# Performance work log

Measured on AMD Instinct MI355X. Metric: run time of the kernel, lower is better.

The kernel has to match this reference:

```python
import jax, jax.numpy as jnp
import numpy as np

N_NODES = 100000
N_EDGES = 1600000
N_REL = 2
IN_CH, HID_CH, OUT_CH = 128, 128, 64


def setup_inputs() -> dict:
    key = jax.random.key(0)
    ks = jax.random.split(key, 8)
    x = jax.random.normal(ks[0], (N_NODES, IN_CH), dtype=jnp.float32)
    edge_index = jax.random.randint(ks[1], (2, N_EDGES), 0, N_NODES, dtype=jnp.int64)
    edge_type = jax.random.randint(ks[2], (N_EDGES,), 0, N_REL, dtype=jnp.int64)
    s1 = 1.0 / np.sqrt(IN_CH)
    s2 = 1.0 / np.sqrt(HID_CH)
    W1_rel = jax.random.normal(ks[3], (N_REL, IN_CH, HID_CH), dtype=jnp.float32) * s1
    W1_root = jax.random.normal(ks[4], (IN_CH, HID_CH), dtype=jnp.float32) * s1
    b1 = jnp.zeros((HID_CH,), dtype=jnp.float32)
    W2_rel = jax.random.normal(ks[5], (N_REL, HID_CH, OUT_CH), dtype=jnp.float32) * s2
    W2_root = jax.random.normal(ks[6], (HID_CH, OUT_CH), dtype=jnp.float32) * s2
    b2 = jnp.zeros((OUT_CH,), dtype=jnp.float32)
    return {"x": x, "edge_index": edge_index, "edge_type": edge_type,
            "W1_rel": W1_rel, "W1_root": W1_root, "b1": b1,
            "W2_rel": W2_rel, "W2_root": W2_root, "b2": b2}


def rgcn_conv(x, edge_index, edge_type, W_rel, W_root, b):
    """Relational graph conv: root transform + per-relation gather/matmul/scatter-mean."""
    src, dst = edge_index[0], edge_index[1]
    N = x.shape[0]
    out = x @ W_root + b  # self/root term
    x_src = x[src]  # [E, in] gather once, reused across relations
    for r in range(W_rel.shape[0]):  # N_REL is small and fixed
        mask = (edge_type == r)
        msg = jnp.where(mask[:, None], x_src, 0.0) @ W_rel[r]  # [E, out]
        agg = jax.ops.segment_sum(msg, dst, num_segments=N)  # [N, out]
        cnt = jax.ops.segment_sum(mask.astype(x.dtype), dst, num_segments=N)
        out = out + agg / jnp.maximum(cnt, 1.0)[:, None]  # mean aggregation
    return out


def l2_normalize(x, eps=1e-12):
    nrm = jnp.sqrt(jnp.sum(x * x, axis=1, keepdims=True))
    return x / jnp.maximum(nrm, eps)


def reference(x, edge_index, edge_type, W1_rel, W1_root, b1, W2_rel, W2_root, b2):
    h = jax.nn.relu(rgcn_conv(x, edge_index, edge_type, W1_rel, W1_root, b1))
    out = rgcn_conv(h, edge_index, edge_type, W2_rel, W2_root, b2)
    return l2_normalize(out)
```

## Files before the change

kernel.cpp:

```cpp
#include <hip/hip_runtime.h>
#include <hip/hip_bf16.h>


typedef unsigned int uint;
typedef unsigned short ushort;
typedef __attribute__((ext_vector_type(8))) short short8;
typedef __attribute__((ext_vector_type(16))) float floatx16;
typedef __attribute__((ext_vector_type(2))) float f32x2;
typedef __attribute__((ext_vector_type(4))) float f32x4;
typedef __attribute__((ext_vector_type(4))) uint u32x4;

#define IN_CH  128
#define OUT_CH 64
#define SCAN_CHUNK 2048
#define EPB 8192
#define KPB 512
#define MAXBK 400

__device__ __forceinline__ ushort f2bf(float f) {
    uint u = __float_as_uint(f);
    u += 0x7FFF + ((u >> 16) & 1);
    return (ushort)(u >> 16);
}
__device__ __forceinline__ float bflo(uint u) { return __uint_as_float(u << 16); }
__device__ __forceinline__ float bfhi(uint u) { return __uint_as_float(u & 0xFFFF0000u); }


__global__ void k_scan_a(const int* __restrict__ deg, int* __restrict__ offs,
                         int* __restrict__ bsums, int n) {
    __shared__ int sdata[256];
    int b = blockIdx.x, t = threadIdx.x;
    int base = b * SCAN_CHUNK + t * 8;
    int v[8];
    int sum = 0;
#pragma unroll
    for (int i = 0; i < 8; i++) {
        int idx = base + i;
        int x = (idx < n) ? deg[idx] : 0;
        v[i] = sum;
        sum += x;
    }
    sdata[t] = sum;
    __syncthreads();
    for (int ofs = 1; ofs < 256; ofs <<= 1) {
        int val = sdata[t];
        int add = (t >= ofs) ? sdata[t - ofs] : 0;
        __syncthreads();
        sdata[t] = val + add;
        __syncthreads();
    }
    int texcl = (t == 0) ? 0 : sdata[t - 1];
    if (t == 255) bsums[b] = sdata[255];
#pragma unroll
    for (int i = 0; i < 8; i++) {
        int idx = base + i;
        if (idx < n) offs[idx] = texcl + v[i];
    }
}

__global__ void k_scan_b(int* __restrict__ bsums, int* __restrict__ offs, int nb, int n) {
    int t = threadIdx.x;
    if (nb <= 64) {
        int v = (t < nb) ? bsums[t] : 0;
        int s = v;
#pragma unroll
        for (int d = 1; d < 64; d <<= 1) {
            int u = __shfl_up(s, d, 64);
            if (t >= d) s += u;
        }
        if (t < nb) bsums[t] = s - v;
        if (t == 63) offs[n] = s;
    } else if (t == 0) {
        int run = 0;
        for (int b = 0; b < nb; b++) {
            int x = bsums[b];
            bsums[b] = run;
            run += x;
        }
        offs[n] = run;
    }
}

__global__ void k_part(const int* __restrict__ src, const int* __restrict__ dst,
                       const int* __restrict__ et, const int* __restrict__ basebb,
                       const int* __restrict__ bsums,
                       uint* __restrict__ stage, int E, int NBK, int NBLK) {
    __shared__ int cnt[MAXBK];
    __shared__ int basel[MAXBK];
    int tid = threadIdx.x, blk = blockIdx.x;
    for (int b = tid; b < NBK; b += 256) {
        cnt[b] = 0;
        int i = b * NBLK + blk;
        basel[b] = basebb[i] + bsums[i >> 11];
    }
    __syncthreads();
    int base = blk * EPB;
#pragma unroll 4
    for (int i = 0; i < EPB / 256; i++) {
        int e = base + i * 256 + tid;
        if (e < E) {
            int s = src[e];
            int key = 2 * dst[e] + et[e];
            int bk = key >> 9;
            int r = atomicAdd(&cnt[bk], 1);
            stage[basel[bk] + r] = ((uint)(key & 511) << 23) | (uint)s;
        }
    }
}

__global__ void k_fine(const uint* __restrict__ stage, const int* __restrict__ basebb,
                       const int* __restrict__ bsums,
                       int* __restrict__ offs, int* __restrict__ esrc,
                       int E, int NBK, int NBLK) {
    __shared__ int kcnt[KPB];
    __shared__ int kcur[KPB];
    __shared__ int ssum[256];
    int tid = threadIdx.x, b = blockIdx.x;
    int i0 = b * NBLK;
    int start = basebb[i0] + bsums[i0 >> 11];
    int endB = E;
    if (b != NBK - 1) {
        int i1 = (b + 1) * NBLK;
        endB = basebb[i1] + bsums[i1 >> 11];
    }
    int size = endB - start;

    kcnt[tid] = 0;
    kcnt[tid + 256] = 0;
    __syncthreads();
    for (int i = tid; i < size; i += 256)
        atomicAdd(&kcnt[stage[start + i] >> 23], 1);
    __syncthreads();
    int v0 = kcnt[2 * tid], v1 = kcnt[2 * tid + 1];
    ssum[tid] = v0 + v1;
    __syncthreads();
    for (int ofs = 1; ofs < 256; ofs <<= 1) {
        int val = ssum[tid];
        int add = (tid >= ofs) ? ssum[tid - ofs] : 0;
        __syncthreads();
        ssum[tid] = val + add;
        __syncthreads();
    }
    int texcl = (tid == 0) ? 0 : ssum[tid - 1];
    kcur[2 * tid] = texcl;
    kcur[2 * tid + 1] = texcl + v0;
    offs[(b << 9) + 2 * tid] = start + texcl + v0;
    offs[(b << 9) + 2 * tid + 1] = start + texcl + v0 + v1;
    __syncthreads();
    for (int i = tid; i < size; i += 256) {
        uint p = stage[start + i];
        int r = atomicAdd(&kcur[p >> 23], 1);
        esrc[start + r] = (int)(p & 0x7FFFFFu);
    }
}


__device__ __forceinline__ uint4 pack8(const ushort* o) {
    uint4 v;
    v.x = (uint)o[0] | ((uint)o[1] << 16);
    v.y = (uint)o[2] | ((uint)o[3] << 16);
    v.z = (uint)o[4] | ((uint)o[5] << 16);
    v.w = (uint)o[6] | ((uint)o[7] << 16);
    return v;
}

__global__ void k_pre(const int* __restrict__ dst, const int* __restrict__ et,
                      int* __restrict__ cntblk, int E, int NBK, int NBLK,
                      const float* __restrict__ x, uint4* __restrict__ xb, int n8,
                      const float* __restrict__ W1root, const float* __restrict__ W1rel,
                      const float* __restrict__ W2root, const float* __restrict__ W2rel,
                      uint4* __restrict__ Bpk1, uint4* __restrict__ Bpk2,
                      uint* __restrict__ xzero, uint* __restrict__ t2zero) {
    __shared__ int cnt[MAXBK];
    int tid = threadIdx.x;
    if ((int)blockIdx.x < NBLK) {
        int blk = blockIdx.x;
        for (int b = tid; b < NBK; b += 256) cnt[b] = 0;
        __syncthreads();
        int base = blk * EPB;
#pragma unroll 4
        for (int i = 0; i < EPB / 256; i++) {
            int e = base + i * 256 + tid;
            if (e < E) {
                int key = 2 * dst[e] + et[e];
                atomicAdd(&cnt[key >> 9], 1);
            }
        }
        __syncthreads();
        for (int b = tid; b < NBK; b += 256) cntblk[b * NBLK + blk] = cnt[b];
        return;
    }
    int bid = blockIdx.x - NBLK;
    if (bid < 40) {
        if (bid == 0) {
            if (tid < 64) xzero[tid] = 0;
            if (tid < 96) t2zero[tid] = 0;
        }
        int idx = bid * 256 + tid;
        ushort o[8];
        if (idx < 6144) {
            int id = idx;
            int ct = id >> 11;
            int c = id & 2047;
            int gn = c >> 9, s = (c >> 6) & 7, h = (c >> 5) & 1, n = c & 31;
            int k0 = s * 16 + h * 8;
            int col = gn * 32 + n;
            const float* W = (ct == 0) ? W1root : (W1rel + (size_t)(ct - 1) * 16384);
#pragma unroll
            for (int j = 0; j < 8; j++) o[j] = f2bf(W[(k0 + j) * 128 + col]);
            Bpk1[id] = pack8(o);
        } else {
            int id = idx - 6144;
            int ct = id >> 11;
            int c = id & 2047;
            int gn = c >> 9, s = (c >> 6) & 7, h = (c >> 5) & 1, n = c & 31;
            int k0 = s * 16 + h * 8;
            int colg = ct * 128 + gn * 32 + n;
#pragma unroll
            for (int j = 0; j < 8; j++) {
                float f = 0.f;
                if (colg < 64)       f = W2root[(k0 + j) * 64 + colg];
                else if (colg < 128) f = W2rel[(k0 + j) * 64 + (colg - 64)];
                else if (colg < 192) f = W2rel[8192 + (k0 + j) * 64 + (colg - 128)];
                o[j] = f2bf(f);
            }
            Bpk2[id] = pack8(o);
        }
    } else {
        int i = (bid - 40) * 256 + tid;
        if (i >= n8) return;
        const f32x4* xp = (const f32x4*)x;
        f32x4 f0 = __builtin_nontemporal_load(&xp[(size_t)i * 2]);
        f32x4 f1 = __builtin_nontemporal_load(&xp[(size_t)i * 2 + 1]);
        uint4 o;
        o.x = (uint)f2bf(f0.x) | ((uint)f2bf(f0.y) << 16);
        o.y = (uint)f2bf(f0.z) | ((uint)f2bf(f0.w) << 16);
        o.z = (uint)f2bf(f1.x) | ((uint)f2bf(f1.y) << 16);
        o.w = (uint)f2bf(f1.z) | ((uint)f2bf(f1.w) << 16);
        xb[i] = o;
    }
}


__global__ __launch_bounds__(256)
void k_agg(const int* __restrict__ offs, const int* __restrict__ esrc,
           const uint4* __restrict__ xb4, uint* __restrict__ S, int N) {
    int wid = (int)((blockIdx.x * 256L + threadIdx.x) >> 5);
    int l = threadIdx.x & 31;
    if (wid >= N) return;
    int q = l >> 4, c = l & 15;

    int beg0 = (wid == 0) ? 0 : offs[2 * wid - 1];
    int end0 = offs[2 * wid], end1 = offs[2 * wid + 1];

    u32x4 o = {0, 0, 0, 0};
#pragma unroll
    for (int r = 0; r < 2; r++) {
        int beg = r ? end0 : beg0;
        int end = r ? end1 : end0;
        f32x2 a0 = {0.f, 0.f}, a1 = {0.f, 0.f}, a2 = {0.f, 0.f}, a3 = {0.f, 0.f};
        for (int c0 = beg; c0 < end; c0 += 32) {
            int myid = (c0 + l < end) ? __builtin_nontemporal_load(&esrc[c0 + l]) : N;
            int m = min(32, end - c0);
            for (int eb = 0; eb < m; eb += 4) {
#pragma unroll
                for (int j = 0; j < 2; j++) {
                    int id = __shfl(myid, eb + 2 * j + q, 32);
                    uint4 v = xb4[(uint)id * 16u + (uint)c];
                    a0 += (f32x2){bflo(v.x), bfhi(v.x)};
                    a1 += (f32x2){bflo(v.y), bfhi(v.y)};
                    a2 += (f32x2){bflo(v.z), bfhi(v.z)};
                    a3 += (f32x2){bflo(v.w), bfhi(v.w)};
                }
            }
        }
        a0.x += __shfl_xor(a0.x, 16, 32); a0.y += __shfl_xor(a0.y, 16, 32);
        a1.x += __shfl_xor(a1.x, 16, 32); a1.y += __shfl_xor(a1.y, 16, 32);
        a2.x += __shfl_xor(a2.x, 16, 32); a2.y += __shfl_xor(a2.y, 16, 32);
        a3.x += __shfl_xor(a3.x, 16, 32); a3.y += __shfl_xor(a3.y, 16, 32);
        if (q == r) {
            float inv = (end > beg) ? 1.0f / (float)(end - beg) : 0.f;
            o.x = (uint)f2bf(a0.x * inv) | ((uint)f2bf(a0.y * inv) << 16);
            o.y = (uint)f2bf(a1.x * inv) | ((uint)f2bf(a1.y * inv) << 16);
            o.z = (uint)f2bf(a2.x * inv) | ((uint)f2bf(a2.y * inv) << 16);
            o.w = (uint)f2bf(a3.x * inv) | ((uint)f2bf(a3.y * inv) << 16);
        }
    }
    u32x4* Sp = (u32x4*)S;
    __builtin_nontemporal_store(o, &Sp[(size_t)wid * 32 + q * 16 + c]);
}


__global__ __launch_bounds__(256)
void k_fused(const ushort* __restrict__ xb, const ushort* __restrict__ S1,
             const ushort* __restrict__ Bpk1, const float* __restrict__ b1,
             const ushort* __restrict__ Bpk2, ushort* __restrict__ Out, int N) {
    __shared__ ushort SH[40960];
    ushort* Alds = SH;
    ushort* Blds = SH + 16384;

    const int tid = threadIdx.x;
    const int lane = tid & 63;
    const int w = tid >> 6;
    const int wm = w >> 1, wn = w & 1;
    const int rowBase = blockIdx.x * 128;

    floatx16 acc[2][2] = {};

#pragma unroll
    for (int seg = 0; seg < 3; seg++) {
        const ushort* Ap = (seg == 0) ? xb : S1;
        const int stride = (seg == 0) ? 128 : 256;
        const int aoff = (seg == 2) ? 128 : 0;
        const uint4* Bsrc = (const uint4*)Bpk1 + seg * 2048;
#pragma unroll
        for (int i = 0; i < 8; i++) {
            int c = tid + i * 256;
            int m = c & 31, hh = (c >> 5) & 1, s = (c >> 6) & 7, g = c >> 9;
            int row = rowBase + g * 32 + m;
            if (row >= N) row = N - 1;
            int kc = s * 2 + hh;
            ((uint4*)Alds)[c] = *(const uint4*)(Ap + (size_t)row * stride + aoff + kc * 8);
            ((uint4*)Blds)[c] = Bsrc[c];
        }
        __syncthreads();
#pragma unroll
        for (int s = 0; s < 8; s++) {
            short8 a0 = *(const short8*)&Alds[(((wm * 2 + 0) * 8 + s) * 64 + lane) * 8];
            short8 a1 = *(const short8*)&Alds[(((wm * 2 + 1) * 8 + s) * 64 + lane) * 8];
            short8 b0 = *(const short8*)&Blds[(((wn * 2 + 0) * 8 + s) * 64 + lane) * 8];
            short8 b1f = *(const short8*)&Blds[(((wn * 2 + 1) * 8 + s) * 64 + lane) * 8];
            acc[0][0] = __builtin_amdgcn_mfma_f32_32x32x16_bf16(a0, b0, acc[0][0], 0, 0, 0);
            acc[0][1] = __builtin_amdgcn_mfma_f32_32x32x16_bf16(a0, b1f, acc[0][1], 0, 0, 0);
            acc[1][0] = __builtin_amdgcn_mfma_f32_32x32x16_bf16(a1, b0, acc[1][0], 0, 0, 0);
            acc[1][1] = __builtin_amdgcn_mfma_f32_32x32x16_bf16(a1, b1f, acc[1][1], 0, 0, 0);
        }
        __syncthreads();
    }

    {
        const int qr = 4 * (lane >> 5);
        const int cl = lane & 31;
        float bb[2];
#pragma unroll
        for (int nt = 0; nt < 2; nt++) bb[nt] = b1[wn * 64 + nt * 32 + cl];
#pragma unroll
        for (int mt = 0; mt < 2; mt++)
#pragma unroll
            for (int nt = 0; nt < 2; nt++) {
                int col = wn * 64 + nt * 32 + cl;
                int kc = col >> 3, j = col & 7;
                int s = kc >> 1, hh = kc & 1;
                int base = (((wm * 2 + mt) * 8 + s) * 64 + hh * 32) * 8 + j;
#pragma unroll
                for (int reg = 0; reg < 16; reg++) {
                    int rl = (reg & 3) + 8 * (reg >> 2) + qr;
                    float v = fmaxf(acc[mt][nt][reg] + bb[nt], 0.f);
                    Alds[base + rl * 8] = f2bf(v);
                }
            }
    }
    {
        const uint4* B2 = (const uint4*)Bpk2;
#pragma unroll
        for (int i = 0; i < 12; i++) {
            int c = tid + i * 256;
            ((uint4*)Blds)[c] = B2[c];
        }
    }
    __syncthreads();

    floatx16 acc2[2][3] = {};
#pragma unroll
    for (int s = 0; s < 8; s++) {
        short8 a0 = *(const short8*)&Alds[(((wm * 2 + 0) * 8 + s) * 64 + lane) * 8];
        short8 a1 = *(const short8*)&Alds[(((wm * 2 + 1) * 8 + s) * 64 + lane) * 8];
        short8 b0 = *(const short8*)&Blds[((wn * 3 + 0) * 512 + s * 64 + lane) * 8];
        short8 b1v = *(const short8*)&Blds[((wn * 3 + 1) * 512 + s * 64 + lane) * 8];
        short8 b2v = *(const short8*)&Blds[((wn * 3 + 2) * 512 + s * 64 + lane) * 8];
        acc2[0][0] = __builtin_amdgcn_mfma_f32_32x32x16_bf16(a0, b0, acc2[0][0], 0, 0, 0);
        acc2[0][1] = __builtin_amdgcn_mfma_f32_32x32x16_bf16(a0, b1v, acc2[0][1], 0, 0, 0);
        acc2[0][2] = __builtin_amdgcn_mfma_f32_32x32x16_bf16(a0, b2v, acc2[0][2], 0, 0, 0);
        acc2[1][0] = __builtin_amdgcn_mfma_f32_32x32x16_bf16(a1, b0, acc2[1][0], 0, 0, 0);
        acc2[1][1] = __builtin_amdgcn_mfma_f32_32x32x16_bf16(a1, b1v, acc2[1][1], 0, 0, 0);
        acc2[1][2] = __builtin_amdgcn_mfma_f32_32x32x16_bf16(a1, b2v, acc2[1][2], 0, 0, 0);
    }
    __syncthreads();

    ushort* Clds = SH;
    {
        const int qr = 4 * (lane >> 5);
        const int cl = lane & 31;
#pragma unroll
        for (int mt = 0; mt < 2; mt++)
#pragma unroll
            for (int nt = 0; nt < 3; nt++) {
#pragma unroll
                for (int reg = 0; reg < 16; reg++) {
                    int rl = (reg & 3) + 8 * (reg >> 2) + qr;
                    Clds[(wm * 64 + mt * 32 + rl) * 200 + wn * 96 + nt * 32 + cl] =
                        f2bf(acc2[mt][nt][reg]);
                }
            }
    }
    __syncthreads();

    int r = tid >> 1, half = tid & 1;
    int grow = rowBase + r;
    if (grow < N) {
#pragma unroll
        for (int k = 0; k < 12; k++) {
            int c0 = half * 96 + k * 8;
            uint4 v = *(const uint4*)&Clds[r * 200 + c0];
            *(uint4*)(Out + (size_t)grow * 192 + c0) = v;
        }
    }
}


__global__ __launch_bounds__(256)
void k_final(const ushort* __restrict__ T2, const float* __restrict__ b2,
             const int* __restrict__ offs, const int* __restrict__ esrc,
             float* __restrict__ out, int N) {
    int wid = (int)((blockIdx.x * 256L + threadIdx.x) >> 3);
    int c = threadIdx.x & 7;
    if (wid >= N) return;
    const uint4* Tb = (const uint4*)T2;

    int beg0 = (wid == 0) ? 0 : offs[2 * wid - 1];
    int end0 = offs[2 * wid], end1 = offs[2 * wid + 1];

    f32x2 t0 = {0.f, 0.f}, t1 = {0.f, 0.f}, t2v = {0.f, 0.f}, t3v = {0.f, 0.f};
#pragma unroll
    for (int r = 0; r < 2; r++) {
        int beg = r ? end0 : beg0;
        int end = r ? end1 : end0;
        if (end > beg) {
            f32x2 a0 = {0.f, 0.f}, a1 = {0.f, 0.f}, a2 = {0.f, 0.f}, a3 = {0.f, 0.f};
            uint bc = 8u + 8u * (uint)r + (uint)c;
            for (int c0 = beg; c0 < end; c0 += 8) {
                int myid = (c0 + c < end) ? __builtin_nontemporal_load(&esrc[c0 + c]) : N;
                int m = min(8, end - c0);
                for (int eb = 0; eb < m; eb += 4) {
                    uint4 v[4];
#pragma unroll
                    for (int j = 0; j < 4; j++) {
                        int id = __shfl(myid, eb + j, 8);
                        v[j] = Tb[(uint)id * 24u + bc];
                    }
#pragma unroll
                    for (int j = 0; j < 4; j++) {
                        a0 += (f32x2){bflo(v[j].x), bfhi(v[j].x)};
                        a1 += (f32x2){bflo(v[j].y), bfhi(v[j].y)};
                        a2 += (f32x2){bflo(v[j].z), bfhi(v[j].z)};
                        a3 += (f32x2){bflo(v[j].w), bfhi(v[j].w)};
                    }
                }
            }
            float inv = 1.0f / (float)(end - beg);
            t0 += a0 * inv; t1 += a1 * inv; t2v += a2 * inv; t3v += a3 * inv;
        }
    }
    uint4 ru = Tb[(uint)wid * 24u + (uint)c];
    float4 bbA = *(const float4*)(b2 + 8 * c);
    float4 bbB = *(const float4*)(b2 + 8 * c + 4);
    float v0 = bflo(ru.x) + bbA.x + t0.x;
    float v1 = bfhi(ru.x) + bbA.y + t0.y;
    float v2 = bflo(ru.y) + bbA.z + t1.x;
    float v3 = bfhi(ru.y) + bbA.w + t1.y;
    float v4 = bflo(ru.z) + bbB.x + t2v.x;
    float v5 = bfhi(ru.z) + bbB.y + t2v.y;
    float v6 = bflo(ru.w) + bbB.z + t3v.x;
    float v7 = bfhi(ru.w) + bbB.w + t3v.y;
    float sq = v0 * v0 + v1 * v1 + v2 * v2 + v3 * v3
             + v4 * v4 + v5 * v5 + v6 * v6 + v7 * v7;
#pragma unroll
    for (int d = 1; d <= 4; d <<= 1) sq += __shfl_xor(sq, d, 8);
    float rn = 1.0f / fmaxf(sqrtf(sq), 1e-12f);
    f32x4 oA = {v0 * rn, v1 * rn, v2 * rn, v3 * rn};
    f32x4 oB = {v4 * rn, v5 * rn, v6 * rn, v7 * rn};
    f32x4* op = (f32x4*)(out + (size_t)wid * 64 + 8 * c);
    __builtin_nontemporal_store(oA, op);
    __builtin_nontemporal_store(oB, op + 1);
}


extern "C" void kernel_launch(void* const* d_in, const int* in_sizes, int n_in,
                              void* d_out, int out_size, void* d_ws, size_t ws_size,
                              hipStream_t stream) {
    const float* x      = (const float*)d_in[0];
    const int*   ei     = (const int*)d_in[1];
    const int*   etype  = (const int*)d_in[2];
    const float* W1rel  = (const float*)d_in[3];
    const float* W1root = (const float*)d_in[4];
    const float* b1     = (const float*)d_in[5];
    const float* W2rel  = (const float*)d_in[6];
    const float* W2root = (const float*)d_in[7];
    const float* b2     = (const float*)d_in[8];
    float* out = (float*)d_out;

    const int N = in_sizes[0] / IN_CH;
    const int E = in_sizes[2];
    const int NKEY = 2 * N;
    const int NBK  = (NKEY + KPB - 1) / KPB;
    const int NBLK = (E + EPB - 1) / EPB;
    const int NSC  = NBK * NBLK;

    const int* src = ei;
    const int* dst = ei + E;

    char* base = (char*)d_ws;
    size_t off = 0;
    auto carve = [&](size_t bytes) -> void* {
        void* p = base + off;
        off = (off + bytes + 511) & ~(size_t)511;
        return p;
    };
    ushort* xb    = (ushort*)carve((size_t)(N + 1) * 128 * sizeof(ushort));
    ushort* S1    = (ushort*)carve((size_t)N * 256 * sizeof(ushort));
    ushort* t2    = (ushort*)carve((size_t)(N + 1) * 192 * sizeof(ushort));
    int*    esrc  = (int*)carve((size_t)E * sizeof(int));
    uint*   stage = (uint*)carve((size_t)E * sizeof(uint));
    int*    offs  = (int*)carve((size_t)NBK * KPB * sizeof(int));
    int*    cntblk= (int*)carve((size_t)NSC * sizeof(int));
    int*    basebb= (int*)carve((size_t)(NSC + 1) * sizeof(int));
    int     NB    = (NSC + SCAN_CHUNK - 1) / SCAN_CHUNK;
    int*    bsums = (int*)carve((size_t)NB * sizeof(int));
    uint4*  Bpk1  = (uint4*)carve(6144 * sizeof(uint4));
    uint4*  Bpk2  = (uint4*)carve(4096 * sizeof(uint4));
    (void)ws_size; (void)n_in; (void)out_size;

    int n8 = N * 16;
    int preBlocks = NBLK + 40 + (n8 + 255) / 256;

    k_pre<<<preBlocks, 256, 0, stream>>>(dst, etype, cntblk, E, NBK, NBLK,
                                         x, (uint4*)xb, n8,
                                         W1root, W1rel, W2root, W2rel,
                                         Bpk1, Bpk2,
                                         (uint*)(xb + (size_t)N * 128),
                                         (uint*)(t2 + (size_t)N * 192));

    k_scan_a<<<NB, 256, 0, stream>>>(cntblk, basebb, bsums, NSC);
    k_scan_b<<<1, 64, 0, stream>>>(bsums, basebb, NB, NSC);
    k_part<<<NBLK, 256, 0, stream>>>(src, dst, etype, basebb, bsums, stage, E, NBK, NBLK);
    k_fine<<<NBK, 256, 0, stream>>>(stage, basebb, bsums, offs, esrc, E, NBK, NBLK);

    int rowTiles = (N + 127) / 128;
    int aggBlocks = (N + 7) / 8;
    int finBlocks = (N + 31) / 32;

    k_agg<<<aggBlocks, 256, 0, stream>>>(offs, esrc, (const uint4*)xb, (uint*)S1, N);
    k_fused<<<rowTiles, 256, 0, stream>>>(xb, S1, (const ushort*)Bpk1, b1,
                                          (const ushort*)Bpk2, t2, N);

    k_final<<<finBlocks, 256, 0, stream>>>(t2, b2, offs, esrc, out, N);
}
```

Before: 330.9 us.

## Read weight fragments from global memory and shrink fused kernel LDS footprint

The fused GEMM kernel no longer stages the packed weight matrices in LDS. Each wave reads its B fragments straight from global memory, where they should stay hot in cache since every block shares them. The output tile is now written back in two 64-row halves so it fits in a 32 KB LDS buffer, down from 80 KB. This is meant to allow more resident blocks per CU and to drop the B staging copies, at the cost of global loads on the MFMA path and extra barriers during writeback.

```diff
diff --git a/kernel.cpp b/kernel.cpp
--- a/kernel.cpp
+++ b/kernel.cpp
@@ -295,9 +295,8 @@
 void k_fused(const ushort* __restrict__ xb, const ushort* __restrict__ S1,
              const ushort* __restrict__ Bpk1, const float* __restrict__ b1,
              const ushort* __restrict__ Bpk2, ushort* __restrict__ Out, int N) {
-    __shared__ ushort SH[40960];
+    __shared__ ushort SH[16384];
     ushort* Alds = SH;
-    ushort* Blds = SH + 16384;
 
     const int tid = threadIdx.x;
     const int lane = tid & 63;
@@ -305,6 +304,9 @@
     const int wm = w >> 1, wn = w & 1;
     const int rowBase = blockIdx.x * 128;
 
+    const short8* B1 = (const short8*)Bpk1;
+    const short8* B2 = (const short8*)Bpk2;
+
     floatx16 acc[2][2] = {};
 
 #pragma unroll
@@ -312,7 +314,6 @@
         const ushort* Ap = (seg == 0) ? xb : S1;
         const int stride = (seg == 0) ? 128 : 256;
         const int aoff = (seg == 2) ? 128 : 0;
-        const uint4* Bsrc = (const uint4*)Bpk1 + seg * 2048;
 #pragma unroll
         for (int i = 0; i < 8; i++) {
             int c = tid + i * 256;
@@ -321,15 +322,14 @@
             if (row >= N) row = N - 1;
             int kc = s * 2 + hh;
             ((uint4*)Alds)[c] = *(const uint4*)(Ap + (size_t)row * stride + aoff + kc * 8);
-            ((uint4*)Blds)[c] = Bsrc[c];
         }
         __syncthreads();
 #pragma unroll
         for (int s = 0; s < 8; s++) {
             short8 a0 = *(const short8*)&Alds[(((wm * 2 + 0) * 8 + s) * 64 + lane) * 8];
             short8 a1 = *(const short8*)&Alds[(((wm * 2 + 1) * 8 + s) * 64 + lane) * 8];
-            short8 b0 = *(const short8*)&Blds[(((wn * 2 + 0) * 8 + s) * 64 + lane) * 8];
-            short8 b1f = *(const short8*)&Blds[(((wn * 2 + 1) * 8 + s) * 64 + lane) * 8];
+            short8 b0 = B1[seg * 2048 + ((wn * 2 + 0) * 8 + s) * 64 + lane];
+            short8 b1f = B1[seg * 2048 + ((wn * 2 + 1) * 8 + s) * 64 + lane];
             acc[0][0] = __builtin_amdgcn_mfma_f32_32x32x16_bf16(a0, b0, acc[0][0], 0, 0, 0);
             acc[0][1] = __builtin_amdgcn_mfma_f32_32x32x16_bf16(a0, b1f, acc[0][1], 0, 0, 0);
             acc[1][0] = __builtin_amdgcn_mfma_f32_32x32x16_bf16(a1, b0, acc[1][0], 0, 0, 0);
@@ -360,14 +360,6 @@
                 }
             }
     }
-    {
-        const uint4* B2 = (const uint4*)Bpk2;
-#pragma unroll
-        for (int i = 0; i < 12; i++) {
-            int c = tid + i * 256;
-            ((uint4*)Blds)[c] = B2[c];
-        }
-    }
     __syncthreads();
 
     floatx16 acc2[2][3] = {};
@@ -375,9 +367,9 @@
     for (int s = 0; s < 8; s++) {
         short8 a0 = *(const short8*)&Alds[(((wm * 2 + 0) * 8 + s) * 64 + lane) * 8];
         short8 a1 = *(const short8*)&Alds[(((wm * 2 + 1) * 8 + s) * 64 + lane) * 8];
-        short8 b0 = *(const short8*)&Blds[((wn * 3 + 0) * 512 + s * 64 + lane) * 8];
-        short8 b1v = *(const short8*)&Blds[((wn * 3 + 1) * 512 + s * 64 + lane) * 8];
-        short8 b2v = *(const short8*)&Blds[((wn * 3 + 2) * 512 + s * 64 + lane) * 8];
+        short8 b0 = B2[((wn * 3 + 0) * 8 + s) * 64 + lane];
+        short8 b1v = B2[((wn * 3 + 1) * 8 + s) * 64 + lane];
+        short8 b2v = B2[((wn * 3 + 2) * 8 + s) * 64 + lane];
         acc2[0][0] = __builtin_amdgcn_mfma_f32_32x32x16_bf16(a0, b0, acc2[0][0], 0, 0, 0);
         acc2[0][1] = __builtin_amdgcn_mfma_f32_32x32x16_bf16(a0, b1v, acc2[0][1], 0, 0, 0);
         acc2[0][2] = __builtin_amdgcn_mfma_f32_32x32x16_bf16(a0, b2v, acc2[0][2], 0, 0, 0);
@@ -385,34 +377,36 @@
         acc2[1][1] = __builtin_amdgcn_mfma_f32_32x32x16_bf16(a1, b1v, acc2[1][1], 0, 0, 0);
         acc2[1][2] = __builtin_amdgcn_mfma_f32_32x32x16_bf16(a1, b2v, acc2[1][2], 0, 0, 0);
     }
-    __syncthreads();
 
     ushort* Clds = SH;
-    {
-        const int qr = 4 * (lane >> 5);
-        const int cl = lane & 31;
-#pragma unroll
-        for (int mt = 0; mt < 2; mt++)
-#pragma unroll
-            for (int nt = 0; nt < 3; nt++) {
-#pragma unroll
-                for (int reg = 0; reg < 16; reg++) {
-                    int rl = (reg & 3) + 8 * (reg >> 2) + qr;
-                    Clds[(wm * 64 + mt * 32 + rl) * 200 + wn * 96 + nt * 32 + cl] =
-                        f2bf(acc2[mt][nt][reg]);
+    const int qr = 4 * (lane >> 5);
+    const int cl = lane & 31;
+#pragma unroll
+    for (int half = 0; half < 2; half++) {
+        __syncthreads();
+        if (wm == half) {
+#pragma unroll
+            for (int mt = 0; mt < 2; mt++)
+#pragma unroll
+                for (int nt = 0; nt < 3; nt++) {
+#pragma unroll
+                    for (int reg = 0; reg < 16; reg++) {
+                        int rl = (reg & 3) + 8 * (reg >> 2) + qr;
+                        Clds[(mt * 32 + rl) * 200 + wn * 96 + nt * 32 + cl] =
+                            f2bf(acc2[mt][nt][reg]);
+                    }
                 }
+        }
+        __syncthreads();
+        int r = tid >> 2, q4 = tid & 3;
+        int grow = rowBase + half * 64 + r;
+        if (grow < N) {
+#pragma unroll
+            for (int k = 0; k < 6; k++) {
+                int c0 = q4 * 48 + k * 8;
+                uint4 v = *(const uint4*)&Clds[r * 200 + c0];
+                *(uint4*)(Out + (size_t)grow * 192 + c0) = v;
             }
-    }
-    __syncthreads();
-
-    int r = tid >> 1, half = tid & 1;
-    int grow = rowBase + r;
-    if (grow < N) {
-#pragma unroll
-        for (int k = 0; k < 12; k++) {
-            int c0 = half * 96 + k * 8;
-            uint4 v = *(const uint4*)&Clds[r * 200 + c0];
-            *(uint4*)(Out + (size_t)grow * 192 + c0) = v;
         }
     }
 }
```

Measured after the change: 338.3 us. 2.2% more time.

## Use 8 waves per block in fused GEMM kernel and plain stores in aggregation

Applied to the files above, without the earlier changes.

The fused two-layer GEMM kernel now launches 512 threads (8 waves) per 128-row tile. Each wave owns one 32-row M tile instead of two, which halves per-wave accumulators and MFMA work and spreads the LDS loads across more threads. This aims to raise latency hiding and reduce register pressure, at the cost of more A-fragment LDS reads relative to compute. The aggregation kernel also switches its S1 output from a nontemporal store to a normal store, so the data may stay in cache for the following fused kernel.

```diff
diff --git a/kernel.cpp b/kernel.cpp
--- a/kernel.cpp
+++ b/kernel.cpp
@@ -244,7 +244,7 @@
 
 __global__ __launch_bounds__(256)
 void k_agg(const int* __restrict__ offs, const int* __restrict__ esrc,
-           const uint4* __restrict__ xb4, uint* __restrict__ S, int N) {
+           const uint4* __restrict__ xb4, uint4* __restrict__ S4, int N) {
     int wid = (int)((blockIdx.x * 256L + threadIdx.x) >> 5);
     int l = threadIdx.x & 31;
     if (wid >= N) return;
@@ -253,7 +253,7 @@
     int beg0 = (wid == 0) ? 0 : offs[2 * wid - 1];
     int end0 = offs[2 * wid], end1 = offs[2 * wid + 1];
 
-    u32x4 o = {0, 0, 0, 0};
+    uint4 o = make_uint4(0, 0, 0, 0);
 #pragma unroll
     for (int r = 0; r < 2; r++) {
         int beg = r ? end0 : beg0;
@@ -286,12 +286,11 @@
             o.w = (uint)f2bf(a3.x * inv) | ((uint)f2bf(a3.y * inv) << 16);
         }
     }
-    u32x4* Sp = (u32x4*)S;
-    __builtin_nontemporal_store(o, &Sp[(size_t)wid * 32 + q * 16 + c]);
-}
-
-
-__global__ __launch_bounds__(256)
+    S4[(size_t)wid * 32 + q * 16 + c] = o;
+}
+
+
+__global__ __launch_bounds__(512)
 void k_fused(const ushort* __restrict__ xb, const ushort* __restrict__ S1,
              const ushort* __restrict__ Bpk1, const float* __restrict__ b1,
              const ushort* __restrict__ Bpk2, ushort* __restrict__ Out, int N) {
@@ -302,10 +301,11 @@
     const int tid = threadIdx.x;
     const int lane = tid & 63;
     const int w = tid >> 6;
-    const int wm = w >> 1, wn = w & 1;
+    const int wm = w & 3;
+    const int wn = w >> 2;
     const int rowBase = blockIdx.x * 128;
 
-    floatx16 acc[2][2] = {};
+    floatx16 acc[2] = {};
 
 #pragma unroll
     for (int seg = 0; seg < 3; seg++) {
@@ -314,8 +314,8 @@
         const int aoff = (seg == 2) ? 128 : 0;
         const uint4* Bsrc = (const uint4*)Bpk1 + seg * 2048;
 #pragma unroll
-        for (int i = 0; i < 8; i++) {
-            int c = tid + i * 256;
+        for (int i = 0; i < 4; i++) {
+            int c = tid + i * 512;
             int m = c & 31, hh = (c >> 5) & 1, s = (c >> 6) & 7, g = c >> 9;
             int row = rowBase + g * 32 + m;
             if (row >= N) row = N - 1;
@@ -326,14 +326,11 @@
         __syncthreads();
 #pragma unroll
         for (int s = 0; s < 8; s++) {
-            short8 a0 = *(const short8*)&Alds[(((wm * 2 + 0) * 8 + s) * 64 + lane) * 8];
-            short8 a1 = *(const short8*)&Alds[(((wm * 2 + 1) * 8 + s) * 64 + lane) * 8];
+            short8 a0 = *(const short8*)&Alds[((wm * 8 + s) * 64 + lane) * 8];
             short8 b0 = *(const short8*)&Blds[(((wn * 2 + 0) * 8 + s) * 64 + lane) * 8];
             short8 b1f = *(const short8*)&Blds[(((wn * 2 + 1) * 8 + s) * 64 + lane) * 8];
-            acc[0][0] = __builtin_amdgcn_mfma_f32_32x32x16_bf16(a0, b0, acc[0][0], 0, 0, 0);
-            acc[0][1] = __builtin_amdgcn_mfma_f32_32x32x16_bf16(a0, b1f, acc[0][1], 0, 0, 0);
-            acc[1][0] = __builtin_amdgcn_mfma_f32_32x32x16_bf16(a1, b0, acc[1][0], 0, 0, 0);
-            acc[1][1] = __builtin_amdgcn_mfma_f32_32x32x16_bf16(a1, b1f, acc[1][1], 0, 0, 0);
+            acc[0] = __builtin_amdgcn_mfma_f32_32x32x16_bf16(a0, b0, acc[0], 0, 0, 0);
+            acc[1] = __builtin_amdgcn_mfma_f32_32x32x16_bf16(a0, b1f, acc[1], 0, 0, 0);
         }
         __syncthreads();
     }
@@ -341,49 +338,39 @@
     {
         const int qr = 4 * (lane >> 5);
         const int cl = lane & 31;
-        float bb[2];
-#pragma unroll
-        for (int nt = 0; nt < 2; nt++) bb[nt] = b1[wn * 64 + nt * 32 + cl];
-#pragma unroll
-        for (int mt = 0; mt < 2; mt++)
-#pragma unroll
-            for (int nt = 0; nt < 2; nt++) {
-                int col = wn * 64 + nt * 32 + cl;
-                int kc = col >> 3, j = col & 7;
-                int s = kc >> 1, hh = kc & 1;
-                int base = (((wm * 2 + mt) * 8 + s) * 64 + hh * 32) * 8 + j;
-#pragma unroll
-                for (int reg = 0; reg < 16; reg++) {
-                    int rl = (reg & 3) + 8 * (reg >> 2) + qr;
-                    float v = fmaxf(acc[mt][nt][reg] + bb[nt], 0.f);
-                    Alds[base + rl * 8] = f2bf(v);
-                }
+#pragma unroll
+        for (int nt = 0; nt < 2; nt++) {
+            float bb = b1[wn * 64 + nt * 32 + cl];
+            int col = wn * 64 + nt * 32 + cl;
+            int kc = col >> 3, j = col & 7;
+            int s = kc >> 1, hh = kc & 1;
+            int base = ((wm * 8 + s) * 64 + hh * 32) * 8 + j;
+#pragma unroll
+            for (int reg = 0; reg < 16; reg++) {
+                int rl = (reg & 3) + 8 * (reg >> 2) + qr;
+                float v = fmaxf(acc[nt][reg] + bb, 0.f);
+                Alds[base + rl * 8] = f2bf(v);
             }
-    }
-    {
-        const uint4* B2 = (const uint4*)Bpk2;
-#pragma unroll
-        for (int i = 0; i < 12; i++) {
-            int c = tid + i * 256;
-            ((uint4*)Blds)[c] = B2[c];
-        }
-    }
-    __syncthreads();
-
-    floatx16 acc2[2][3] = {};
+        }
+        const uint4* B2s = (const uint4*)Bpk2;
+#pragma unroll
+        for (int i = 0; i < 6; i++) {
+            int c = tid + i * 512;
+            ((uint4*)Blds)[c] = B2s[c];
+        }
+    }
+    __syncthreads();
+
+    floatx16 acc2[3] = {};
 #pragma unroll
     for (int s = 0; s < 8; s++) {
-        short8 a0 = *(const short8*)&Alds[(((wm * 2 + 0) * 8 + s) * 64 + lane) * 8];
-        short8 a1 = *(const short8*)&Alds[(((wm * 2 + 1) * 8 + s) * 64 + lane) * 8];
-        short8 b0 = *(const short8*)&Blds[((wn * 3 + 0) * 512 + s * 64 + lane) * 8];
-        short8 b1v = *(const short8*)&Blds[((wn * 3 + 1) * 512 + s * 64 + lane) * 8];
-        short8 b2v = *(const short8*)&Blds[((wn * 3 + 2) * 512 + s * 64 + lane) * 8];
-        acc2[0][0] = __builtin_amdgcn_mfma_f32_32x32x16_bf16(a0, b0, acc2[0][0], 0, 0, 0);
-        acc2[0][1] = __builtin_amdgcn_mfma_f32_32x32x16_bf16(a0, b1v, acc2[0][1], 0, 0, 0);
-        acc2[0][2] = __builtin_amdgcn_mfma_f32_32x32x16_bf16(a0, b2v, acc2[0][2], 0, 0, 0);
-        acc2[1][0] = __builtin_amdgcn_mfma_f32_32x32x16_bf16(a1, b0, acc2[1][0], 0, 0, 0);
-        acc2[1][1] = __builtin_amdgcn_mfma_f32_32x32x16_bf16(a1, b1v, acc2[1][1], 0, 0, 0);
-        acc2[1][2] = __builtin_amdgcn_mfma_f32_32x32x16_bf16(a1, b2v, acc2[1][2], 0, 0, 0);
+        short8 a0 = *(const short8*)&Alds[((wm * 8 + s) * 64 + lane) * 8];
+        short8 b0 = *(const short8*)&Blds[(((wn * 3 + 0) * 8 + s) * 64 + lane) * 8];
+        short8 b1v = *(const short8*)&Blds[(((wn * 3 + 1) * 8 + s) * 64 + lane) * 8];
+        short8 b2v = *(const short8*)&Blds[(((wn * 3 + 2) * 8 + s) * 64 + lane) * 8];
+        acc2[0] = __builtin_amdgcn_mfma_f32_32x32x16_bf16(a0, b0, acc2[0], 0, 0, 0);
+        acc2[1] = __builtin_amdgcn_mfma_f32_32x32x16_bf16(a0, b1v, acc2[1], 0, 0, 0);
+        acc2[2] = __builtin_amdgcn_mfma_f32_32x32x16_bf16(a0, b2v, acc2[2], 0, 0, 0);
     }
     __syncthreads();
 
@@ -392,25 +379,23 @@
         const int qr = 4 * (lane >> 5);
         const int cl = lane & 31;
 #pragma unroll
-        for (int mt = 0; mt < 2; mt++)
-#pragma unroll
-            for (int nt = 0; nt < 3; nt++) {
-#pragma unroll
-                for (int reg = 0; reg < 16; reg++) {
-                    int rl = (reg & 3) + 8 * (reg >> 2) + qr;
-                    Clds[(wm * 64 + mt * 32 + rl) * 200 + wn * 96 + nt * 32 + cl] =
-                        f2bf(acc2[mt][nt][reg]);
-                }
+        for (int nt = 0; nt < 3; nt++) {
+#pragma unroll
+            for (int reg = 0; reg < 16; reg++) {
+                int rl = (reg & 3) + 8 * (reg >> 2) + qr;
+                Clds[(wm * 32 + rl) * 200 + wn * 96 + nt * 32 + cl] =
+                    f2bf(acc2[nt][reg]);
             }
-    }
-    __syncthreads();
-
-    int r = tid >> 1, half = tid & 1;
+        }
+    }
+    __syncthreads();
+
+    int r = tid >> 2, q4 = tid & 3;
     int grow = rowBase + r;
     if (grow < N) {
 #pragma unroll
-        for (int k = 0; k < 12; k++) {
-            int c0 = half * 96 + k * 8;
+        for (int k = 0; k < 6; k++) {
+            int c0 = q4 * 48 + k * 8;
             uint4 v = *(const uint4*)&Clds[r * 200 + c0];
             *(uint4*)(Out + (size_t)grow * 192 + c0) = v;
         }
@@ -549,8 +534,8 @@
     int aggBlocks = (N + 7) / 8;
     int finBlocks = (N + 31) / 32;
 
-    k_agg<<<aggBlocks, 256, 0, stream>>>(offs, esrc, (const uint4*)xb, (uint*)S1, N);
-    k_fused<<<rowTiles, 256, 0, stream>>>(xb, S1, (const ushort*)Bpk1, b1,
+    k_agg<<<aggBlocks, 256, 0, stream>>>(offs, esrc, (const uint4*)xb, (uint4*)S1, N);
+    k_fused<<<rowTiles, 512, 0, stream>>>(xb, S1, (const ushort*)Bpk1, b1,
                                           (const ushort*)Bpk2, t2, N);
 
     k_final<<<finBlocks, 256, 0, stream>>>(t2, b2, offs, esrc, out, N);
```

Result: faster. 310.4 us (-6.2%).
